# Performance work log

Hardware: AMD Instinct MI355X
Metric: run time of the kernel (lower is better)

Reference implementation:

```python
import jax, jax.numpy as jnp
import numpy as np

N, C, H, W = 16, 64, 128, 128
SHIFT = 1  # frozen value of torch module's random.randint(-2, 2) drawn at __init__


def setup_inputs() -> dict:
    key = jax.random.key(0)
    k1, k2, k3 = jax.random.split(key, 3)
    x = jax.random.normal(k1, (N, C, H, W), dtype=jnp.float32)
    # p_3: Conv2d(c, c, (1,5), padding=(0,2), bias=False) -> weight (C_out, C_in, 1, 5)
    w3 = jax.random.normal(k2, (C, C, 1, 5), dtype=jnp.float32) * (1.0 / np.sqrt(5.0 * C))
    # p_7: Conv2d(9c, c, 1, groups=c, bias=False) -> per output channel, 9 input channels: (C, 9)
    w7 = jax.random.normal(k3, (C, 9), dtype=jnp.float32) * (1.0 / 3.0)
    return {"x": x, "w3": w3, "w7": w7}


def reference(x, w3, w7):
    n, c, h, w = x.shape
    # t_1: F.unfold(x, (1,3), dilation=(1,2), padding=(0,2)) -> width offsets -2, 0, +2 (zero padded)
    xp = jnp.pad(x, ((0, 0), (0, 0), (0, 0), (2, 2)))
    t1 = jnp.stack([xp[..., 0:w], xp[..., 2:w + 2], xp[..., 4:w + 4]], axis=2)  # (n,c,3,h,w)
    # t_3: 1x5 conv, padding (0,2)
    t3 = jax.lax.conv_general_dilated(
        x, w3, window_strides=(1, 1), padding=[(0, 0), (2, 2)],
        dimension_numbers=("NCHW", "OIHW", "NCHW"))  # (n,c,h,w)
    # t_4: F.unfold(t1 as (n,3c,h,w), (3,1), padding=(1,0)) -> height offsets -1, 0, +1
    t1p = jnp.pad(t1, ((0, 0), (0, 0), (0, 0), (1, 1), (0, 0)))
    t4 = jnp.stack([t1p[..., 0:h, :], t1p[..., 1:h + 1, :], t1p[..., 2:h + 2, :]],
                   axis=3)  # (n, c, 3[w_off], 3[h_off], h, w)
    # t_5: roll along the W axis (dim 5)
    t5 = jnp.roll(t4, SHIFT, axis=5)
    # t_6: maximum of lhs (n,c,1,3,h,w) and rhs (n,c,3,3,h,w); lhs offset dim aligns with rhs dim 3
    t6 = jnp.maximum(t1[:, :, None, :, :, :], t5)  # (n,c,3,3,h,w)
    # t_7: grouped 1x1 conv, groups=c, 9 input channels per group -> 1 output channel
    t6f = t6.reshape(n, c, 9, h, w)
    t7 = jnp.einsum("nckhw,ck->nchw", t6f, w7)
    return t7 * t3
```

## Files before the change

### kernel.cpp

```cpp
#include <hip/hip_runtime.h>

#define NN 16
#define CC 64
#define HH 128
#define WW 128

#define LDS_STRIDE 72

typedef __attribute__((ext_vector_type(8))) short short8;
typedef __attribute__((ext_vector_type(4))) float floatx4;

__device__ __forceinline__ short f2bf(float f) {
    union { float f; unsigned u; } v; v.f = f;
    unsigned r = v.u + 0x7fffu + ((v.u >> 16) & 1u);
    return (short)(r >> 16);
}

__global__ __launch_bounds__(256) void prep_w(const float* __restrict__ w3,
                                              short* __restrict__ Abf) {
    int idx = blockIdx.x * 256 + threadIdx.x;
    if (idx < CC * CC * 5) {
        int tap = idx % 5;
        int ci  = (idx / 5) % CC;
        int co  = idx / (5 * CC);
        Abf[co * 320 + tap * 64 + ci] = f2bf(w3[idx]);
    }
}

__global__ __launch_bounds__(256) void conv_mfma(const float* __restrict__ x,
                                                 const short* __restrict__ Abf,
                                                 float* __restrict__ t3) {
    __shared__ short xsT[132 * LDS_STRIDE];
    const int nh  = blockIdx.x;
    const int n   = nh >> 7;
    const int h   = nh & (HH - 1);
    const int tid = threadIdx.x;

    const float* xbase = x + (((size_t)n * CC) * HH + h) * WW;
    #pragma unroll
    for (int i = 0; i < 8; ++i) {
        int idx = tid + i * 256;
        int ci  = idx >> 5;
        int wq  = idx & 31;
        float4 v = *(const float4*)(xbase + (size_t)ci * (HH * WW) + wq * 4);
        int wp = wq * 4 + 2;
        xsT[(wp + 0) * LDS_STRIDE + ci] = f2bf(v.x);
        xsT[(wp + 1) * LDS_STRIDE + ci] = f2bf(v.y);
        xsT[(wp + 2) * LDS_STRIDE + ci] = f2bf(v.z);
        xsT[(wp + 3) * LDS_STRIDE + ci] = f2bf(v.w);
    }
    {
        int wpi = tid >> 6;
        int wpz = (wpi < 2) ? wpi : 128 + wpi;
        int ci  = tid & 63;
        xsT[wpz * LDS_STRIDE + ci] = 0;
    }
    __syncthreads();

    const int W    = tid >> 6;
    const int lane = tid & 63;
    const int lm   = lane & 15;
    const int g    = lane >> 4;

    floatx4 acc[8];
    #pragma unroll
    for (int nt = 0; nt < 8; ++nt) acc[nt] = (floatx4){0.f, 0.f, 0.f, 0.f};

    const short* arow = Abf + (W * 16 + lm) * 320;

    for (int ks = 0; ks < 10; ++ks) {
        const int kbase = ks * 32 + g * 8;
        const int tap   = kbase >> 6;
        const int cib   = kbase & 63;

        short8 a = *(const short8*)(arow + kbase);
        #pragma unroll
        for (int nt = 0; nt < 8; ++nt) {
            int wp = nt * 16 + lm + tap;
            short8 b = *(const short8*)&xsT[wp * LDS_STRIDE + cib];
            acc[nt] = __builtin_amdgcn_mfma_f32_16x16x32_bf16(a, b, acc[nt], 0, 0, 0);
        }
    }

    #pragma unroll
    for (int nt = 0; nt < 8; ++nt) {
        #pragma unroll
        for (int r = 0; r < 4; ++r) {
            int co = W * 16 + g * 4 + r;
            t3[(((size_t)n * CC + co) * HH + h) * WW + nt * 16 + lm] = acc[nt][r];
        }
    }
}

__global__ __launch_bounds__(256) void combine4(const float* __restrict__ x,
                                                const float* __restrict__ t3,
                                                const float* __restrict__ w7,
                                                float* __restrict__ out) {
    const int tid4 = blockIdx.x * 256 + threadIdx.x;
    const int flat = tid4 * 4;
    const int w0 = flat & (WW - 1);
    const int h  = (flat >> 7) & (HH - 1);
    const int nc = flat >> 14;
    const int c  = nc & (CC - 1);
    const float* xb = x + (size_t)nc * (HH * WW);

    float win[3][12];
    #pragma unroll
    for (int r = 0; r < 3; ++r) {
        int hh = h + r - 1;
        bool hok = (unsigned)hh < HH;
        #pragma unroll
        for (int q = 0; q < 3; ++q) {
            int cb = w0 - 4 + q * 4;
            float4 v = make_float4(0.f, 0.f, 0.f, 0.f);
            if (hok && (unsigned)cb < WW)
                v = *(const float4*)(xb + hh * WW + cb);
            win[r][q * 4 + 0] = v.x; win[r][q * 4 + 1] = v.y;
            win[r][q * 4 + 2] = v.z; win[r][q * 4 + 3] = v.w;
        }
    }
    float wrap0[3] = {0.f, 0.f, 0.f}, wrap1[3] = {0.f, 0.f, 0.f};
    if (w0 == 0) {
        #pragma unroll
        for (int r = 0; r < 3; ++r) {
            int hh = h + r - 1;
            if ((unsigned)hh < HH) {
                wrap0[r] = xb[hh * WW + 125];
                wrap1[r] = xb[hh * WW + 127];
            }
        }
    }
    float wc[9];
    #pragma unroll
    for (int t = 0; t < 9; ++t) wc[t] = w7[c * 9 + t];

    float4 t3v = *(const float4*)(t3 + flat);
    float res[4];
    #pragma unroll
    for (int e = 0; e < 4; ++e) {
        float acc = 0.f;
        #pragma unroll
        for (int j = 0; j < 3; ++j) {
            #pragma unroll
            for (int i = 0; i < 3; ++i) {
                float lhs = win[1][e + 2 * i + 2];
                float rhs;
                if (e == 0 && w0 == 0)
                    rhs = (j == 0) ? wrap0[i] : ((j == 1) ? wrap1[i] : 0.f);
                else
                    rhs = win[i][e + 2 * j + 1];
                acc = fmaf(wc[j * 3 + i], fmaxf(lhs, rhs), acc);
            }
        }
        res[e] = acc;
    }
    float4 o;
    o.x = res[0] * t3v.x; o.y = res[1] * t3v.y;
    o.z = res[2] * t3v.z; o.w = res[3] * t3v.w;
    *(float4*)(out + flat) = o;
}

extern "C" void kernel_launch(void* const* d_in, const int* in_sizes, int n_in,
                              void* d_out, int out_size, void* d_ws, size_t ws_size,
                              hipStream_t stream) {
    const float* x  = (const float*)d_in[0];
    const float* w3 = (const float*)d_in[1];
    const float* w7 = (const float*)d_in[2];
    float* out = (float*)d_out;

    float* t3  = (float*)d_ws;
    short* Abf = (short*)(t3 + (size_t)NN * CC * HH * WW);

    prep_w<<<(CC * CC * 5 + 255) / 256, 256, 0, stream>>>(w3, Abf);
    conv_mfma<<<NN * HH, 256, 0, stream>>>(x, Abf, t3);
    combine4<<<(NN * CC * HH * WW) / (4 * 256), 256, 0, stream>>>(x, t3, w7, out);
}
```

Baseline: 160.5 us.

## Fuse MFMA conv and combine into one kernel via shared-memory t3

Merges the 1x5 MFMA convolution and the max/grouped-conv combine stage into a single kernel per (n,h) row. The conv result is staged in LDS (reusing the input buffer) instead of being written to and re-read from a global t3 workspace, which removes a full-size intermediate round trip through HBM and one kernel launch. The trade-off is a larger LDS footprint per block (about 33 KB), which may lower occupancy, plus extra barriers. The combine stage now reads x with a per-channel stride inside each block, which may change access locality.

```diff
diff --git a/kernel.cpp b/kernel.cpp
--- a/kernel.cpp
+++ b/kernel.cpp
@@ -6,6 +6,7 @@
 #define WW 128
 
 #define LDS_STRIDE 72
+#define T3_STRIDE 132
 
 typedef __attribute__((ext_vector_type(8))) short short8;
 typedef __attribute__((ext_vector_type(4))) float floatx4;
@@ -27,10 +28,14 @@
     }
 }
 
-__global__ __launch_bounds__(256) void conv_mfma(const float* __restrict__ x,
-                                                 const short* __restrict__ Abf,
-                                                 float* __restrict__ t3) {
-    __shared__ short xsT[132 * LDS_STRIDE];
+__global__ __launch_bounds__(256) void fused(const float* __restrict__ x,
+                                             const short* __restrict__ Abf,
+                                             const float* __restrict__ w7,
+                                             float* __restrict__ out) {
+    __shared__ __align__(16) char smem[CC * T3_STRIDE * 4];
+    short* xsT = (short*)smem;
+    float* t3s = (float*)smem;
+
     const int nh  = blockIdx.x;
     const int n   = nh >> 7;
     const int h   = nh & (HH - 1);
@@ -81,83 +86,82 @@
             acc[nt] = __builtin_amdgcn_mfma_f32_16x16x32_bf16(a, b, acc[nt], 0, 0, 0);
         }
     }
+    __syncthreads();
 
     #pragma unroll
     for (int nt = 0; nt < 8; ++nt) {
         #pragma unroll
         for (int r = 0; r < 4; ++r) {
             int co = W * 16 + g * 4 + r;
-            t3[(((size_t)n * CC + co) * HH + h) * WW + nt * 16 + lm] = acc[nt][r];
+            t3s[co * T3_STRIDE + nt * 16 + lm] = acc[nt][r];
         }
     }
-}
+    __syncthreads();
 
-__global__ __launch_bounds__(256) void combine4(const float* __restrict__ x,
-                                                const float* __restrict__ t3,
-                                                const float* __restrict__ w7,
-                                                float* __restrict__ out) {
-    const int tid4 = blockIdx.x * 256 + threadIdx.x;
-    const int flat = tid4 * 4;
-    const int w0 = flat & (WW - 1);
-    const int h  = (flat >> 7) & (HH - 1);
-    const int nc = flat >> 14;
-    const int c  = nc & (CC - 1);
-    const float* xb = x + (size_t)nc * (HH * WW);
+    float* orow = out + (((size_t)n * CC) * HH + h) * WW;
+    #pragma unroll
+    for (int it = 0; it < 8; ++it) {
+        const int item = it * 256 + tid;
+        const int flat = item * 4;
+        const int w0   = flat & (WW - 1);
+        const int c    = flat >> 7;
+        const float* xb = x + ((size_t)(n * CC + c) * HH) * WW;
 
-    float win[3][12];
-    #pragma unroll
-    for (int r = 0; r < 3; ++r) {
-        int hh = h + r - 1;
-        bool hok = (unsigned)hh < HH;
-        #pragma unroll
-        for (int q = 0; q < 3; ++q) {
-            int cb = w0 - 4 + q * 4;
-            float4 v = make_float4(0.f, 0.f, 0.f, 0.f);
-            if (hok && (unsigned)cb < WW)
-                v = *(const float4*)(xb + hh * WW + cb);
-            win[r][q * 4 + 0] = v.x; win[r][q * 4 + 1] = v.y;
-            win[r][q * 4 + 2] = v.z; win[r][q * 4 + 3] = v.w;
-        }
-    }
-    float wrap0[3] = {0.f, 0.f, 0.f}, wrap1[3] = {0.f, 0.f, 0.f};
-    if (w0 == 0) {
+        float win[3][12];
         #pragma unroll
         for (int r = 0; r < 3; ++r) {
             int hh = h + r - 1;
-            if ((unsigned)hh < HH) {
-                wrap0[r] = xb[hh * WW + 125];
-                wrap1[r] = xb[hh * WW + 127];
+            bool hok = (unsigned)hh < HH;
+            #pragma unroll
+            for (int q = 0; q < 3; ++q) {
+                int cb = w0 - 4 + q * 4;
+                float4 v = make_float4(0.f, 0.f, 0.f, 0.f);
+                if (hok && (unsigned)cb < WW)
+                    v = *(const float4*)(xb + hh * WW + cb);
+                win[r][q * 4 + 0] = v.x; win[r][q * 4 + 1] = v.y;
+                win[r][q * 4 + 2] = v.z; win[r][q * 4 + 3] = v.w;
             }
         }
-    }
-    float wc[9];
-    #pragma unroll
-    for (int t = 0; t < 9; ++t) wc[t] = w7[c * 9 + t];
-
-    float4 t3v = *(const float4*)(t3 + flat);
-    float res[4];
-    #pragma unroll
-    for (int e = 0; e < 4; ++e) {
-        float acc = 0.f;
-        #pragma unroll
-        for (int j = 0; j < 3; ++j) {
+        float wrap0[3] = {0.f, 0.f, 0.f}, wrap1[3] = {0.f, 0.f, 0.f};
+        if (w0 == 0) {
             #pragma unroll
-            for (int i = 0; i < 3; ++i) {
-                float lhs = win[1][e + 2 * i + 2];
-                float rhs;
-                if (e == 0 && w0 == 0)
-                    rhs = (j == 0) ? wrap0[i] : ((j == 1) ? wrap1[i] : 0.f);
-                else
-                    rhs = win[i][e + 2 * j + 1];
-                acc = fmaf(wc[j * 3 + i], fmaxf(lhs, rhs), acc);
+            for (int r = 0; r < 3; ++r) {
+                int hh = h + r - 1;
+                if ((unsigned)hh < HH) {
+                    wrap0[r] = xb[hh * WW + 125];
+                    wrap1[r] = xb[hh * WW + 127];
+                }
             }
         }
-        res[e] = acc;
+        float wc[9];
+        #pragma unroll
+        for (int t = 0; t < 9; ++t) wc[t] = w7[c * 9 + t];
+
+        float4 t3v = *(const float4*)&t3s[c * T3_STRIDE + w0];
+        float res[4];
+        #pragma unroll
+        for (int e = 0; e < 4; ++e) {
+            float a = 0.f;
+            #pragma unroll
+            for (int j = 0; j < 3; ++j) {
+                #pragma unroll
+                for (int i = 0; i < 3; ++i) {
+                    float lhs = win[1][e + 2 * i + 2];
+                    float rhs;
+                    if (e == 0 && w0 == 0)
+                        rhs = (j == 0) ? wrap0[i] : ((j == 1) ? wrap1[i] : 0.f);
+                    else
+                        rhs = win[i][e + 2 * j + 1];
+                    a = fmaf(wc[j * 3 + i], fmaxf(lhs, rhs), a);
+                }
+            }
+            res[e] = a;
+        }
+        float4 o;
+        o.x = res[0] * t3v.x; o.y = res[1] * t3v.y;
+        o.z = res[2] * t3v.z; o.w = res[3] * t3v.w;
+        *(float4*)(orow + (size_t)c * (HH * WW) + w0) = o;
     }
-    float4 o;
-    o.x = res[0] * t3v.x; o.y = res[1] * t3v.y;
-    o.z = res[2] * t3v.z; o.w = res[3] * t3v.w;
-    *(float4*)(out + flat) = o;
 }
 
 extern "C" void kernel_launch(void* const* d_in, const int* in_sizes, int n_in,
@@ -168,10 +172,8 @@
     const float* w7 = (const float*)d_in[2];
     float* out = (float*)d_out;
 
-    float* t3  = (float*)d_ws;
-    short* Abf = (short*)(t3 + (size_t)NN * CC * HH * WW);
+    short* Abf = (short*)d_ws;
 
     prep_w<<<(CC * CC * 5 + 255) / 256, 256, 0, stream>>>(w3, Abf);
-    conv_mfma<<<NN * HH, 256, 0, stream>>>(x, Abf, t3);
-    combine4<<<(NN * CC * HH * WW) / (4 * 256), 256, 0, stream>>>(x, t3, w7, out);
+    fused<<<NN * HH, 256, 0, stream>>>(x, Abf, w7, out);
 }
```

Result: faster. 154.2 us (-3.9%).
